# Performance work log

Measured on AMD Instinct MI355X. Metric: run time of the kernel, lower is better.

The kernel has to match this reference:

```python
import jax, jax.numpy as jnp
import numpy as np


def conv_transpose_4s2p1(x, w, b):
    # torch ConvTranspose2d(k=4, s=2, p=1). w is torch layout [Cin, Cout, 4, 4].
    # Equivalent to a regular conv with lhs_dilation=2, per-side pad k-1-p=2,
    # spatially-flipped kernel and in/out channels swapped.
    wk = jnp.flip(w, (2, 3)).transpose(1, 0, 2, 3)  # [Cout, Cin, 4, 4]
    y = jax.lax.conv_general_dilated(
        x, wk, window_strides=(1, 1), padding=((2, 2), (2, 2)),
        lhs_dilation=(2, 2), dimension_numbers=('NCHW', 'OIHW', 'NCHW'))
    return y + b[None, :, None, None]


def pac_conv_transpose_3s1p1(y, guide, w, b):
    # PacConvTranspose2d(k=3, s=1, p=1): with stride 1 this equals pacconv2d on
    # input zero-padded by k-1-p = 1, with the weight in/out-permuted and flipped
    # (pacnet native impl). Adaptive kernel: K_kk = exp(-0.5*||g_nbr - g_center||^2)
    # computed on the (zero-padded) guide at output resolution.
    B, C, H, W = y.shape
    wk = jnp.flip(w, (2, 3)).transpose(1, 0, 2, 3)  # [Cout, Cin, 3, 3]
    Co = wk.shape[0]
    gp = jnp.pad(guide, ((0, 0), (0, 0), (1, 1), (1, 1)))
    yp = jnp.pad(y, ((0, 0), (0, 0), (1, 1), (1, 1)))
    out = jnp.zeros((B, Co, H, W), y.dtype)
    for i in range(3):  # fixed 3x3 taps, not a data-dim loop
        for j in range(3):
            gn = gp[:, :, i:i + H, j:j + W]                # [B,Cg,H,W] neighbor
            d = gn - guide
            k = jnp.exp(-0.5 * jnp.sum(d * d, axis=1))      # [B,H,W] gaussian kernel
            yn = yp[:, :, i:i + H, j:j + W]                # [B,C,H,W]
            out = out + jnp.einsum('oc,bchw->bohw', wk[:, :, i, j], yn * k[:, None])
    return out + b[None, :, None, None]


def setup_inputs() -> dict:
    key = jax.random.key(0)
    k1, k2, k3, k4, k5, k6 = jax.random.split(key, 6)
    B, Cin, Cout, H, W = 4, 256, 128, 64, 64
    x = jax.random.normal(k1, (B, Cin, H, W), jnp.float32)
    # guide scaled so ||diff||^2 over 128 channels stays O(1-10) and the
    # gaussian kernel is not numerically degenerate
    guide = 0.08 * jax.random.normal(k2, (B, Cout, 2 * H, 2 * W), jnp.float32)
    w1 = jax.random.normal(k3, (Cin, Cout, 4, 4), jnp.float32) / np.sqrt(Cin * 16)
    b1 = 0.01 * jax.random.normal(k4, (Cout,), jnp.float32)
    w2 = jax.random.normal(k5, (Cout, Cout, 3, 3), jnp.float32) / np.sqrt(Cout * 9)
    b2 = 0.01 * jax.random.normal(k6, (Cout,), jnp.float32)
    return {'x': x, 'guide': guide, 'w1': w1, 'b1': b1, 'w2': w2, 'b2': b2}


def reference(x, guide, w1, b1, w2, b2):
    y = conv_transpose_4s2p1(x, w1, b1)          # [B, Cout, 2H, 2W]
    out = pac_conv_transpose_3s1p1(y, guide, w2, b2)
    return out
```

## Files before the change

### kernel.cpp

```cpp
#include <hip/hip_runtime.h>

#define B_  4
#define C1  256
#define C2  128
#define HH  64
#define WW  64
#define H2  128
#define W2  128

using short8  = __attribute__((ext_vector_type(8))) short;
using floatx4 = __attribute__((ext_vector_type(4))) float;
typedef unsigned short ushort_t;

#define GLOBAL_AS __attribute__((address_space(1)))
#define LDS_AS    __attribute__((address_space(3)))

#define W1C_OFF 0u
#define W1C_ELEMS (4 * 4 * 128 * 256)
#define W2C_OFF (W1C_ELEMS * 2u)
#define W2C_ELEMS (9 * 128 * 128)
#define KG_OFF  (W2C_OFF + W2C_ELEMS * 2u)
#define KG_ELEMS (B_ * H2 * 9 * W2)
#define XT_OFF  (KG_OFF + KG_ELEMS * 4u)
#define XT_ELEMS (B_ * HH * WW * C1)
#define Y_OFF   (XT_OFF + XT_ELEMS * 2u)
#define Y_ELEMS (B_ * H2 * W2 * C2)

static __device__ __forceinline__ ushort_t f2bf(float f) {
    union { float f; unsigned u; } v; v.f = f;
    unsigned r = v.u + 0x7FFFu + ((v.u >> 16) & 1u);
    return (ushort_t)(r >> 16);
}

__global__ void w1c_kernel(const float* __restrict__ w1, ushort_t* __restrict__ w1c) {
    int i = blockIdx.x * 256 + threadIdx.x;
    const int sub = i & 7;
    const int gs  = (i >> 3) & 7;
    const int co  = (i >> 6) & 127;
    const int pwp = (i >> 13) & 1;
    const int p   = (i >> 14) & 1;
    const int tap = (i >> 15) & 3;
    const int kc  = (i >> 17) & 3;
    const int ci  = kc * 64 + (((gs ^ (co & 7)) << 3) | sub);
    const int kh  = p + 2 * (tap >> 1);
    const int kw  = pwp + 2 * (tap & 1);
    w1c[i] = f2bf(w1[((ci * C2 + co) * 4 + kh) * 4 + kw]);
}

__global__ void w2c_kernel(const float* __restrict__ w2, ushort_t* __restrict__ w2c) {
    int i = blockIdx.x * 256 + threadIdx.x;
    const int ci  = i & 127;
    const int o   = (i >> 7) & 127;
    const int tap = i >> 14;
    const int fi  = 2 - tap / 3;
    const int fj  = 2 - tap % 3;
    const int gs  = ((((ci >> 3) ^ (o & 7)) << 3) | (ci & 7));
    w2c[tap * 16384 + o * 128 + gs] = f2bf(w2[((ci * C2 + o) * 3 + fi) * 3 + fj]);
}

__global__ __launch_bounds__(256) void xt_kernel(const float* __restrict__ x,
                                                 ushort_t* __restrict__ xT) {
    const int ih = blockIdx.x;
    const int b  = blockIdx.y;
    const int tid = threadIdx.x;
    __shared__ ushort_t tile[64 * 72];

    for (int chunk = 0; chunk < 4; ++chunk) {
        const int ci0 = chunk * 64;
        if (chunk) __syncthreads();
#pragma unroll
        for (int it = 0; it < 16; ++it) {
            const int cc = it * 4 + (tid >> 6);
            const int iw = tid & 63;
            const float v = x[(((size_t)b * C1 + ci0 + cc) * HH + ih) * WW + iw];
            tile[iw * 72 + cc] = f2bf(v);
        }
        __syncthreads();
#pragma unroll
        for (int it = 0; it < 2; ++it) {
            const int i  = it * 256 + tid;
            const int iw = i >> 3;
            const int t  = i & 7;
            const int4 v = *reinterpret_cast<const int4*>(&tile[iw * 72 + t * 8]);
            *reinterpret_cast<int4*>(&xT[(((size_t)(b * HH + ih) * WW) + iw) * C1 + ci0 + t * 8]) = v;
        }
    }
}

__global__ __launch_bounds__(512) void k_kernel(const float* __restrict__ guide,
                                                float* __restrict__ kg) {
    const int h = blockIdx.x;
    const int b = blockIdx.y;
    const int tid = threadIdx.x;
    const int cq  = tid >> 7;
    const int n   = tid & 127;

    float acc[9];
#pragma unroll
    for (int t = 0; t < 9; ++t) acc[t] = 0.f;

    const float* gb = guide + (size_t)b * C2 * H2 * W2;
    for (int c = cq * 32; c < cq * 32 + 32; ++c) {
        const float* grow = gb + (c * H2 + h) * W2;
        const float gc = grow[n];
#pragma unroll
        for (int di = 0; di < 3; ++di) {
            const int hh = h + di - 1;
            const bool rv = (hh >= 0) && (hh < H2);
            const float* gr = gb + (c * H2 + (rv ? hh : 0)) * W2;
#pragma unroll
            for (int dj = 0; dj < 3; ++dj) {
                const int col = n + dj - 1;
                const bool cv = rv && (col >= 0) && (col < W2);
                const float gn = cv ? gr[col] : 0.f;
                const float d = gn - gc;
                acc[di * 3 + dj] += d * d;
            }
        }
    }

    __shared__ float part[4][9][128];
#pragma unroll
    for (int t = 0; t < 9; ++t) part[cq][t][n] = acc[t];
    __syncthreads();

    for (int i = tid; i < 1152; i += 512) {
        const int t  = i >> 7;
        const int nn = i & 127;
        const float s = part[0][t][nn] + part[1][t][nn] + part[2][t][nn] + part[3][t][nn];
        kg[(size_t)(b * H2 + h) * 1152 + i] = __expf(-0.5f * s);
    }
}

__global__ __launch_bounds__(512, 2) void deconv_mfma(const ushort_t* __restrict__ xT,
                                                      const ushort_t* __restrict__ w1s,
                                                      const float* __restrict__ b1,
                                                      ushort_t* __restrict__ y) {
    const int pr = blockIdx.x;
    const int b  = blockIdx.y;
    const int base_oh = (pr >> 1) * 4 + (pr & 1);
    const int p    = (base_oh + 1) & 1;
    const int ihA0 = (base_oh + 1 - p) >> 1;

    const int tid  = threadIdx.x;
    const int lane = tid & 63;
    const int wave = tid >> 6;
    const int pwc  = wave >> 2;
    const int q    = wave & 3;
    const int wm   = (q & 1) * 64;
    const int wn   = (q >> 1) * 64;
    const int quad = lane >> 4;
    const int l15  = lane & 15;
    const int pwp  = 1 - pwc;

    __shared__ __align__(16) ushort_t BS[3 * 64 * 256];
    __shared__ __align__(16) ushort_t AS[2][2 * 128 * 64];

    {
        const ushort_t* src = w1s + (size_t)(0 * 2 + p) * 16384;
#pragma unroll
        for (int it = 0; it < 4; ++it) {
            const int i = it * 512 + tid;
            __builtin_amdgcn_global_load_lds((const GLOBAL_AS void*)(src + i * 8),
                                             (LDS_AS void*)(&AS[0][i * 8]), 16, 0, 0);
        }
    }
#pragma unroll
    for (int it = 0; it < 12; ++it) {
        const int i   = it * 512 + tid;
        const int pix = i >> 5;
        const int g   = i & 31;
        const int sr  = pix >> 6;
        const int iw  = pix & 63;
        const int ih  = ihA0 - 1 + sr;
        int4 v = make_int4(0, 0, 0, 0);
        if (ih >= 0 && ih < HH)
            v = *reinterpret_cast<const int4*>(
                &xT[(((size_t)(b * HH + ih) * WW) + iw) * C1 + g * 8]);
        *reinterpret_cast<int4*>(&BS[pix * 256 + ((g ^ (pix & 7)) << 3)]) = v;
    }
    __syncthreads();

    floatx4 acc[4][4];
#pragma unroll
    for (int mi = 0; mi < 4; ++mi)
#pragma unroll
        for (int ni = 0; ni < 4; ++ni) acc[mi][ni] = (floatx4)0.f;

#pragma unroll 1
    for (int ph = 0; ph < 16; ++ph) {
        const int kc  = ph >> 2;
        const int tap = ph & 3;
        const int cur = ph & 1;
        if (ph < 15) {
            const ushort_t* src = w1s + (size_t)((ph + 1) * 2 + p) * 16384;
#pragma unroll
            for (int it = 0; it < 4; ++it) {
                const int i = it * 512 + tid;
                __builtin_amdgcn_global_load_lds((const GLOBAL_AS void*)(src + i * 8),
                                                 (LDS_AS void*)(&AS[cur ^ 1][i * 8]), 16, 0, 0);
            }
        }
        const int th = tap >> 1, tw = tap & 1;
#pragma unroll
        for (int k2 = 0; k2 < 2; ++k2) {
            short8 af[4], bfr[4];
#pragma unroll
            for (int mi = 0; mi < 4; ++mi) {
                const int row = wm + mi * 16 + l15;
                af[mi] = *reinterpret_cast<const short8*>(
                    &AS[cur][pwp * 8192 + row * 64 + (((k2 * 4 + quad) ^ (row & 7)) << 3)]);
            }
#pragma unroll
            for (int ni = 0; ni < 4; ++ni) {
                const int n   = wn + ni * 16 + l15;
                const int rh  = n >> 6;
                const int n64 = n & 63;
                const int iw  = n64 + pwc - tw;
                const int pix = (rh - th + 1) * 64 + (iw & 63);
                const short8 t = *reinterpret_cast<const short8*>(
                    &BS[pix * 256 + kc * 64 + (((k2 * 4 + quad) ^ (pix & 7)) << 3)]);
                const bool ok = (iw >= 0) && (iw < WW);
                bfr[ni] = ok ? t : (short8)0;
            }
#pragma unroll
            for (int mi = 0; mi < 4; ++mi)
#pragma unroll
                for (int ni = 0; ni < 4; ++ni)
                    acc[mi][ni] = __builtin_amdgcn_mfma_f32_16x16x32_bf16(
                        af[mi], bfr[ni], acc[mi][ni], 0, 0, 0);
        }
        __syncthreads();
    }

    ushort_t* Ot = BS;
#pragma unroll
    for (int mi = 0; mi < 4; ++mi)
#pragma unroll
        for (int ni = 0; ni < 4; ++ni) {
            const int n = wn + ni * 16 + l15;
#pragma unroll
            for (int r = 0; r < 4; ++r) {
                const int co = wm + mi * 16 + quad * 4 + r;
                Ot[(pwc * 128 + n) * 136 + co] = f2bf(acc[mi][ni][r] + b1[co]);
            }
        }
    __syncthreads();
#pragma unroll
    for (int it = 0; it < 8; ++it) {
        const int i    = it * 512 + tid;
        const int n_   = i >> 4;
        const int t    = i & 15;
        const int half = n_ >> 7;
        const int n    = n_ & 127;
        const int rh   = n >> 6;
        const int n64  = n & 63;
        const int oh   = base_oh + 2 * rh;
        const int ow   = 2 * n64 + half;
        const int4 v = *reinterpret_cast<const int4*>(&Ot[n_ * 136 + t * 8]);
        *reinterpret_cast<int4*>(&y[(((size_t)(b * H2 + oh) * W2) + ow) * C2 + t * 8]) = v;
    }
}

__global__ __launch_bounds__(512, 2) void pac_mfma(const ushort_t* __restrict__ y,
                                                   const float* __restrict__ kg,
                                                   const ushort_t* __restrict__ w2c,
                                                   const float* __restrict__ b2,
                                                   float* __restrict__ out) {
    const int hblk = blockIdx.x;
    const int b    = blockIdx.y;
    const int h0   = hblk * 2;

    const int tid  = threadIdx.x;
    const int lane = tid & 63;
    const int wave = tid >> 6;
    const int rsub = wave >> 2;
    const int q    = wave & 3;
    const int wm   = (q & 1) * 64;
    const int wn   = (q >> 1) * 64;
    const int quad = lane >> 4;
    const int l15  = lane & 15;
    const int h    = h0 + rsub;

    __shared__ __align__(16) ushort_t SLAB[4][128 * 128];
    __shared__ __align__(16) ushort_t AS[128 * 128];

#pragma unroll 1
    for (int s = 0; s < 4; ++s) {
        const int hh = h0 - 1 + s;
        if (hh < 0 || hh >= H2) continue;
        const ushort_t* ysrc = y + (size_t)(b * H2 + hh) * W2 * C2;
#pragma unroll
        for (int it = 0; it < 4; ++it) {
            const int i = it * 512 + tid;
            const int w = i >> 4;
            const int c = i & 15;
            const int4 v = *reinterpret_cast<const int4*>(&ysrc[i * 8]);
            *reinterpret_cast<int4*>(&SLAB[s][w * 128 + ((c ^ (w & 7)) << 3)]) = v;
        }
    }
#pragma unroll
    for (int it = 0; it < 4; ++it) {
        const int i = it * 512 + tid;
        __builtin_amdgcn_global_load_lds((const GLOBAL_AS void*)(w2c + i * 8),
                                         (LDS_AS void*)(&AS[i * 8]), 16, 0, 0);
    }
    __syncthreads();

    float out_acc[4][4][4];
#pragma unroll
    for (int mi = 0; mi < 4; ++mi)
#pragma unroll
        for (int ni = 0; ni < 4; ++ni)
#pragma unroll
            for (int r = 0; r < 4; ++r) out_acc[mi][ni][r] = 0.f;

#pragma unroll 1
    for (int di = 0; di < 3; ++di) {
        const int hh  = h + di - 1;
        const bool hok = (hh >= 0) && (hh < H2);
        const ushort_t* SB = &SLAB[rsub + di][0];
#pragma unroll 1
        for (int dj = 0; dj < 3; ++dj) {
            const int tap = di * 3 + dj;

            float kv[4];
#pragma unroll
            for (int ni = 0; ni < 4; ++ni)
                kv[ni] = kg[(size_t)(b * H2 + h) * 1152 + tap * 128 + wn + ni * 16 + l15];

            floatx4 acc[4][4];
#pragma unroll
            for (int mi = 0; mi < 4; ++mi)
#pragma unroll
                for (int ni = 0; ni < 4; ++ni) acc[mi][ni] = (floatx4)0.f;

#pragma unroll
            for (int kc = 0; kc < 4; ++kc) {
                short8 af[4], bfr[4];
#pragma unroll
                for (int mi = 0; mi < 4; ++mi) {
                    const int row = wm + mi * 16 + l15;
                    af[mi] = *reinterpret_cast<const short8*>(
                        &AS[row * 128 + (((kc * 4 + quad) ^ (row & 7)) << 3)]);
                }
#pragma unroll
                for (int ni = 0; ni < 4; ++ni) {
                    const int col  = wn + ni * 16 + l15 + dj - 1;
                    const int colc = col & 127;
                    const short8 t = *reinterpret_cast<const short8*>(
                        &SB[colc * 128 + (((kc * 4 + quad) ^ (colc & 7)) << 3)]);
                    const bool ok = hok && (col >= 0) && (col < W2);
                    bfr[ni] = ok ? t : (short8)0;
                }
#pragma unroll
                for (int mi = 0; mi < 4; ++mi)
#pragma unroll
                    for (int ni = 0; ni < 4; ++ni)
                        acc[mi][ni] = __builtin_amdgcn_mfma_f32_16x16x32_bf16(
                            af[mi], bfr[ni], acc[mi][ni], 0, 0, 0);
            }
#pragma unroll
            for (int mi = 0; mi < 4; ++mi)
#pragma unroll
                for (int ni = 0; ni < 4; ++ni)
#pragma unroll
                    for (int r = 0; r < 4; ++r)
                        out_acc[mi][ni][r] += kv[ni] * acc[mi][ni][r];

            if (tap < 8) {
                __syncthreads();
                const ushort_t* wsrc = w2c + (size_t)(tap + 1) * 16384;
#pragma unroll
                for (int it = 0; it < 4; ++it) {
                    const int i = it * 512 + tid;
                    __builtin_amdgcn_global_load_lds((const GLOBAL_AS void*)(wsrc + i * 8),
                                                     (LDS_AS void*)(&AS[i * 8]), 16, 0, 0);
                }
                __syncthreads();
            }
        }
    }

#pragma unroll
    for (int mi = 0; mi < 4; ++mi)
#pragma unroll
        for (int ni = 0; ni < 4; ++ni) {
            const int w = wn + ni * 16 + l15;
#pragma unroll
            for (int r = 0; r < 4; ++r) {
                const int o = wm + mi * 16 + quad * 4 + r;
                out[(((size_t)b * C2 + o) * H2 + h) * W2 + w] = out_acc[mi][ni][r] + b2[o];
            }
        }
}

extern "C" void kernel_launch(void* const* d_in, const int* in_sizes, int n_in,
                              void* d_out, int out_size, void* d_ws, size_t ws_size,
                              hipStream_t stream) {
    const float* x     = (const float*)d_in[0];
    const float* guide = (const float*)d_in[1];
    const float* w1    = (const float*)d_in[2];
    const float* b1    = (const float*)d_in[3];
    const float* w2    = (const float*)d_in[4];
    const float* b2    = (const float*)d_in[5];
    float* out = (float*)d_out;

    ushort_t* w1c = (ushort_t*)((char*)d_ws + W1C_OFF);
    ushort_t* w2c = (ushort_t*)((char*)d_ws + W2C_OFF);
    float*    kg  = (float*)((char*)d_ws + KG_OFF);
    ushort_t* xT  = (ushort_t*)((char*)d_ws + XT_OFF);
    ushort_t* y   = (ushort_t*)((char*)d_ws + Y_OFF);

    w1c_kernel<<<W1C_ELEMS / 256, 256, 0, stream>>>(w1, w1c);
    w2c_kernel<<<W2C_ELEMS / 256, 256, 0, stream>>>(w2, w2c);
    xt_kernel<<<dim3(HH, B_), 256, 0, stream>>>(x, xT);
    k_kernel<<<dim3(H2, B_), 512, 0, stream>>>(guide, kg);
    deconv_mfma<<<dim3(64, B_), 512, 0, stream>>>(xT, w1c, b1, y);
    pac_mfma<<<dim3(64, B_), 512, 0, stream>>>(y, kg, w2c, b2, out);
}
```

Measured before the change: 184.3 us.

## Double-buffer PAC weight taps and rotate guide slab rows via async LDS loads

The first kernel now writes y with its channel chunks XOR-swizzled in global memory, so the PAC kernel can load y rows straight into LDS with global_load_lds instead of staging them through registers. The weight tile for the next tap is prefetched into a second LDS buffer while the current tap computes, which cuts the two barriers per tap down to one. The y slab drops from 4 rows to a 3-row ring, and the fourth row is loaded into the freed slot during di==1. Loads now overlap with MFMA work, in exchange for subtler buffer-reuse correctness: row hh>=H2 is no longer zeroed, and the code relies on the hok mask to ignore it.

```diff
diff --git a/kernel.cpp b/kernel.cpp
--- a/kernel.cpp
+++ b/kernel.cpp
@@ -258,7 +258,8 @@
         const int oh   = base_oh + 2 * rh;
         const int ow   = 2 * n64 + half;
         const int4 v = *reinterpret_cast<const int4*>(&Ot[n_ * 136 + t * 8]);
-        *reinterpret_cast<int4*>(&y[(((size_t)(b * H2 + oh) * W2) + ow) * C2 + t * 8]) = v;
+        *reinterpret_cast<int4*>(
+            &y[(((size_t)(b * H2 + oh) * W2) + ow) * C2 + ((t ^ (ow & 7)) << 3)]) = v;
     }
 }
 
@@ -282,28 +283,26 @@
     const int l15  = lane & 15;
     const int h    = h0 + rsub;
 
-    __shared__ __align__(16) ushort_t SLAB[4][128 * 128];
-    __shared__ __align__(16) ushort_t AS[128 * 128];
-
-#pragma unroll 1
-    for (int s = 0; s < 4; ++s) {
-        const int hh = h0 - 1 + s;
-        if (hh < 0 || hh >= H2) continue;
-        const ushort_t* ysrc = y + (size_t)(b * H2 + hh) * W2 * C2;
-#pragma unroll
-        for (int it = 0; it < 4; ++it) {
-            const int i = it * 512 + tid;
-            const int w = i >> 4;
-            const int c = i & 15;
-            const int4 v = *reinterpret_cast<const int4*>(&ysrc[i * 8]);
-            *reinterpret_cast<int4*>(&SLAB[s][w * 128 + ((c ^ (w & 7)) << 3)]) = v;
-        }
-    }
+    __shared__ __align__(16) ushort_t SLAB[3][128 * 128];
+    __shared__ __align__(16) ushort_t AS[2][128 * 128];
+
 #pragma unroll
     for (int it = 0; it < 4; ++it) {
         const int i = it * 512 + tid;
         __builtin_amdgcn_global_load_lds((const GLOBAL_AS void*)(w2c + i * 8),
-                                         (LDS_AS void*)(&AS[i * 8]), 16, 0, 0);
+                                         (LDS_AS void*)(&AS[0][i * 8]), 16, 0, 0);
+    }
+#pragma unroll 1
+    for (int s = 0; s < 3; ++s) {
+        const int hh = h0 - 1 + s;
+        if (hh < 0) continue;
+        const ushort_t* ysrc = y + (size_t)(b * H2 + hh) * W2 * C2;
+#pragma unroll
+        for (int it = 0; it < 4; ++it) {
+            const int i = it * 512 + tid;
+            __builtin_amdgcn_global_load_lds((const GLOBAL_AS void*)(ysrc + i * 8),
+                                             (LDS_AS void*)(&SLAB[s][i * 8]), 16, 0, 0);
+        }
     }
     __syncthreads();
 
@@ -317,12 +316,31 @@
 
 #pragma unroll 1
     for (int di = 0; di < 3; ++di) {
+        if (di == 1 && h0 + 2 < H2) {
+            const ushort_t* ysrc = y + (size_t)(b * H2 + h0 + 2) * W2 * C2;
+#pragma unroll
+            for (int it = 0; it < 4; ++it) {
+                const int i = it * 512 + tid;
+                __builtin_amdgcn_global_load_lds((const GLOBAL_AS void*)(ysrc + i * 8),
+                                                 (LDS_AS void*)(&SLAB[0][i * 8]), 16, 0, 0);
+            }
+        }
         const int hh  = h + di - 1;
         const bool hok = (hh >= 0) && (hh < H2);
-        const ushort_t* SB = &SLAB[rsub + di][0];
+        const ushort_t* SB = &SLAB[(rsub + di) % 3][0];
 #pragma unroll 1
         for (int dj = 0; dj < 3; ++dj) {
             const int tap = di * 3 + dj;
+            if (tap < 8) {
+                const ushort_t* wsrc = w2c + (size_t)(tap + 1) * 16384;
+#pragma unroll
+                for (int it = 0; it < 4; ++it) {
+                    const int i = it * 512 + tid;
+                    __builtin_amdgcn_global_load_lds((const GLOBAL_AS void*)(wsrc + i * 8),
+                                                     (LDS_AS void*)(&AS[(tap + 1) & 1][i * 8]),
+                                                     16, 0, 0);
+                }
+            }
 
             float kv[4];
 #pragma unroll
@@ -335,6 +353,7 @@
 #pragma unroll
                 for (int ni = 0; ni < 4; ++ni) acc[mi][ni] = (floatx4)0.f;
 
+            const ushort_t* AScur = &AS[tap & 1][0];
 #pragma unroll
             for (int kc = 0; kc < 4; ++kc) {
                 short8 af[4], bfr[4];
@@ -342,7 +361,7 @@
                 for (int mi = 0; mi < 4; ++mi) {
                     const int row = wm + mi * 16 + l15;
                     af[mi] = *reinterpret_cast<const short8*>(
-                        &AS[row * 128 + (((kc * 4 + quad) ^ (row & 7)) << 3)]);
+                        &AScur[row * 128 + (((kc * 4 + quad) ^ (row & 7)) << 3)]);
                 }
 #pragma unroll
                 for (int ni = 0; ni < 4; ++ni) {
@@ -368,17 +387,7 @@
                     for (int r = 0; r < 4; ++r)
                         out_acc[mi][ni][r] += kv[ni] * acc[mi][ni][r];
 
-            if (tap < 8) {
-                __syncthreads();
-                const ushort_t* wsrc = w2c + (size_t)(tap + 1) * 16384;
-#pragma unroll
-                for (int it = 0; it < 4; ++it) {
-                    const int i = it * 512 + tid;
-                    __builtin_amdgcn_global_load_lds((const GLOBAL_AS void*)(wsrc + i * 8),
-                                                     (LDS_AS void*)(&AS[i * 8]), 16, 0, 0);
-                }
-                __syncthreads();
-            }
+            __syncthreads();
         }
     }
 
```

Result: no change. 183.3 us (-0.5%).
